# Performance work log

Measured on AMD Instinct MI355X. Metric: run time of the kernel, lower is better.

Reference implementation:

```python
import jax, jax.numpy as jnp
import numpy as np

EMBED = 768
HEADS = 12
HEAD_DIM = EMBED // HEADS
HIDDEN = 4 * EMBED
EPS = 1e-5


def _layernorm(x, g, b):
    mu = jnp.mean(x, axis=-1, keepdims=True)
    var = jnp.var(x, axis=-1, keepdims=True)
    return (x - mu) * jax.lax.rsqrt(var + EPS) * g + b


def setup_inputs() -> dict:
    key = jax.random.key(0)
    ks = jax.random.split(key, 12)
    s_e = 1.0 / np.sqrt(EMBED)
    s_h = 1.0 / np.sqrt(HIDDEN)
    return {
        "x": jax.random.normal(ks[0], (2, 2048, EMBED), dtype=jnp.float32),
        "ln1_g": jnp.ones((EMBED,), jnp.float32),
        "ln1_b": jnp.zeros((EMBED,), jnp.float32),
        "qkv_w": jax.random.uniform(ks[1], (EMBED, 3 * EMBED), jnp.float32, -s_e, s_e),
        "qkv_b": jax.random.uniform(ks[2], (3 * EMBED,), jnp.float32, -s_e, s_e),
        "proj_w": jax.random.uniform(ks[3], (EMBED, EMBED), jnp.float32, -s_e, s_e),
        "proj_b": jax.random.uniform(ks[4], (EMBED,), jnp.float32, -s_e, s_e),
        "ln2_g": jnp.ones((EMBED,), jnp.float32),
        "ln2_b": jnp.zeros((EMBED,), jnp.float32),
        "fc1_w": jax.random.uniform(ks[5], (EMBED, HIDDEN), jnp.float32, -s_e, s_e),
        "fc1_b": jax.random.uniform(ks[6], (HIDDEN,), jnp.float32, -s_e, s_e),
        "fc2_w": jax.random.uniform(ks[7], (HIDDEN, EMBED), jnp.float32, -s_h, s_h),
        "fc2_b": jax.random.uniform(ks[8], (EMBED,), jnp.float32, -s_h, s_h),
    }


def reference(x, ln1_g, ln1_b, qkv_w, qkv_b, proj_w, proj_b,
              ln2_g, ln2_b, fc1_w, fc1_b, fc2_w, fc2_b):
    B, L, C = x.shape
    scale = HEAD_DIM ** -0.5

    # --- attention sublayer (pre-LN) ---
    h = _layernorm(x, ln1_g, ln1_b)
    qkv = h @ qkv_w + qkv_b                       # [B, L, 3C]
    qkv = qkv.reshape(B, L, 3, HEADS, HEAD_DIM)
    q = jnp.transpose(qkv[:, :, 0], (0, 2, 1, 3))  # [B, H, L, D]
    k = jnp.transpose(qkv[:, :, 1], (0, 2, 1, 3))
    v = jnp.transpose(qkv[:, :, 2], (0, 2, 1, 3))
    attn = jnp.einsum('bhqd,bhkd->bhqk', q, k) * scale  # [B, H, L, L]
    attn = jax.nn.softmax(attn, axis=-1)
    out = jnp.einsum('bhqk,bhkd->bhqd', attn, v)  # [B, H, L, D]
    out = jnp.transpose(out, (0, 2, 1, 3)).reshape(B, L, C)
    x = x + (out @ proj_w + proj_b)

    # --- FFN sublayer (pre-LN) ---
    h = _layernorm(x, ln2_g, ln2_b)
    h = jax.nn.gelu(h @ fc1_w + fc1_b, approximate=False)
    x = x + (h @ fc2_w + fc2_b)
    return x
```

## Files before the change

kernel.cpp:

```cpp
#include <hip/hip_runtime.h>
#include <hip/hip_bf16.h>
#include <math.h>

#define EMBED   768
#define NHEADS  12
#define HD      64
#define HIDDEN  3072
#define SEQ     2048
#define BATCH   2
#define ROWS    (BATCH*SEQ)

#define QSCALE  0.1803368801111204f

typedef __bf16 bf16_t;
typedef __attribute__((ext_vector_type(8))) __bf16 bf16x8;
typedef __attribute__((ext_vector_type(4))) float f32x4;

static __device__ __forceinline__ f32x4 mfma16(bf16x8 a, bf16x8 b, f32x4 c) {
  return __builtin_amdgcn_mfma_f32_16x16x32_bf16(a, b, c, 0, 0, 0);
}

typedef __attribute__((address_space(1))) const void gas_void;
typedef __attribute__((address_space(3))) void las_void;
static __device__ __forceinline__ void gll16(const void* g, void* l) {
  __builtin_amdgcn_global_load_lds((gas_void*)g, (las_void*)l, 16, 0, 0);
}

__global__ __launch_bounds__(256) void ln_kernel(
    const float* __restrict__ x, const float* __restrict__ g,
    const float* __restrict__ bt, bf16_t* __restrict__ out)
{
  int row = blockIdx.x;
  int tid = threadIdx.x;
  const float* xr = x + (size_t)row * EMBED;
  float v0 = xr[tid], v1 = xr[tid + 256], v2 = xr[tid + 512];
  float s  = v0 + v1 + v2;
  float s2 = v0*v0 + v1*v1 + v2*v2;
  #pragma unroll
  for (int o = 32; o >= 1; o >>= 1) {
    s  += __shfl_xor(s,  o, 64);
    s2 += __shfl_xor(s2, o, 64);
  }
  __shared__ float red[8];
  int wave = tid >> 6, lane = tid & 63;
  if (lane == 0) { red[wave] = s; red[wave + 4] = s2; }
  __syncthreads();
  s  = red[0] + red[1] + red[2] + red[3];
  s2 = red[4] + red[5] + red[6] + red[7];
  float mu  = s * (1.0f / EMBED);
  float var = s2 * (1.0f / EMBED) - mu * mu;
  float rs  = rsqrtf(var + 1e-5f);
  bf16_t* orow = out + (size_t)row * EMBED;
  orow[tid]       = (bf16_t)((v0 - mu) * rs * g[tid]       + bt[tid]);
  orow[tid + 256] = (bf16_t)((v1 - mu) * rs * g[tid + 256] + bt[tid + 256]);
  orow[tid + 512] = (bf16_t)((v2 - mu) * rs * g[tid + 512] + bt[tid + 512]);
}

__global__ __launch_bounds__(256) void transpose_cast(
    const float* __restrict__ in, bf16_t* __restrict__ out, int R, int C)
{
  __shared__ float tile[32][33];
  int c0 = blockIdx.x * 32, r0 = blockIdx.y * 32;
  int tx = threadIdx.x & 31, ty = threadIdx.x >> 5;
  #pragma unroll
  for (int p = 0; p < 4; ++p) {
    int r = ty + p * 8;
    tile[r][tx] = in[(size_t)(r0 + r) * C + c0 + tx];
  }
  __syncthreads();
  #pragma unroll
  for (int p = 0; p < 4; ++p) {
    int cc = ty + p * 8;
    out[(size_t)(c0 + cc) * R + r0 + tx] = (bf16_t)tile[tx][cc];
  }
}

__global__ __launch_bounds__(256) void v_transpose(
    const bf16_t* __restrict__ qkv, bf16_t* __restrict__ vt)
{
  __shared__ bf16_t tile[64][68];
  int bh = blockIdx.y;
  int b = bh / NHEADS, h = bh % NHEADS;
  int l0 = blockIdx.x * 64;
  int t = threadIdx.x;
  int dx = (t & 15) * 4;
  int ly = t >> 4;
  #pragma unroll
  for (int p = 0; p < 4; ++p) {
    int l = ly + p * 16;
    const bf16_t* src = qkv + (size_t)(b * SEQ + l0 + l) * 2304 + 1536 + h * HD + dx;
    *(uint2*)&tile[l][dx] = *(const uint2*)src;
  }
  __syncthreads();
  int lx = (t & 15) * 4;
  int dy = t >> 4;
  #pragma unroll
  for (int p = 0; p < 4; ++p) {
    int d = dy + p * 16;
    union { bf16_t h4[4]; uint2 u; } tmp;
    #pragma unroll
    for (int i = 0; i < 4; ++i) tmp.h4[i] = tile[lx + i][d];
    *(uint2*)&vt[((size_t)bh * HD + d) * SEQ + l0 + lx] = tmp.u;
  }
}

template<int MODE, int BN>
__global__ __launch_bounds__(256) void gemm_kernel(
    const bf16_t* __restrict__ A, const bf16_t* __restrict__ WT,
    const float* __restrict__ bias, const float* __restrict__ res,
    void* __restrict__ outp, int N, int K)
{
  constexpr int JT = BN / 32;
  __shared__ bf16_t As[128 * 64];
  __shared__ bf16_t Bs[BN * 64];
  int tid = threadIdx.x;
  int lane = tid & 63, wave = tid >> 6;
  int l15 = lane & 15, quad = lane >> 4;
  int wm = wave >> 1, wn = wave & 1;

  int Nn = N / BN;
  int lin = blockIdx.x;
  int bm = (lin & 7) + 8 * ((lin >> 3) / Nn);
  int bn = (lin >> 3) % Nn;
  int m0 = bm * 128, n0 = bn * BN;

  f32x4 acc[4][JT];
  #pragma unroll
  for (int i = 0; i < 4; ++i)
    #pragma unroll
    for (int j = 0; j < JT; ++j)
      acc[i][j] = (f32x4){0.f, 0.f, 0.f, 0.f};

  int grow = lane >> 3;
  int gcol = ((lane & 7) ^ grow) * 8;
  const bf16_t* abase = A  + (size_t)(m0 + wave * 32 + grow) * K + gcol;
  const bf16_t* bbase = WT + (size_t)(n0 + wave * (BN / 4) + grow) * K + gcol;
  int swk = l15 & 7;

  for (int k0 = 0; k0 < K; k0 += 64) {
    #pragma unroll
    for (int a = 0; a < 4; ++a)
      gll16(abase + (size_t)a * 8 * K + k0, &As[(wave * 32 + a * 8) * 64]);
    #pragma unroll
    for (int a = 0; a < BN / 32; ++a)
      gll16(bbase + (size_t)a * 8 * K + k0, &Bs[(wave * (BN / 4) + a * 8) * 64]);
    __syncthreads();

    #pragma unroll
    for (int g = 0; g < 2; ++g) {
      bf16x8 af[4], bfr[JT];
      #pragma unroll
      for (int i = 0; i < 4; ++i)
        af[i] = *(const bf16x8*)
            &As[(wm * 64 + i * 16 + l15) * 64 + (((g * 4 + quad) ^ swk) * 8)];
      #pragma unroll
      for (int j = 0; j < JT; ++j)
        bfr[j] = *(const bf16x8*)
            &Bs[(wn * (BN / 2) + j * 16 + l15) * 64 + (((g * 4 + quad) ^ swk) * 8)];
      #pragma unroll
      for (int i = 0; i < 4; ++i)
        #pragma unroll
        for (int j = 0; j < JT; ++j)
          acc[i][j] = mfma16(af[i], bfr[j], acc[i][j]);
    }
    __syncthreads();
  }

  #pragma unroll
  for (int i = 0; i < 4; ++i) {
    int mbase = m0 + wm * 64 + i * 16 + quad * 4;
    #pragma unroll
    for (int j = 0; j < JT; ++j) {
      int n = n0 + wn * (BN / 2) + j * 16 + l15;
      float bn_ = bias[n];
      #pragma unroll
      for (int r = 0; r < 4; ++r) {
        size_t idx = (size_t)(mbase + r) * N + n;
        float v = acc[i][j][r] + bn_;
        if (MODE == 1) v = 0.5f * v * (1.0f + erff(v * 0.70710678118654752f));
        if (MODE == 3 && n < 768) v *= QSCALE;
        if (MODE == 2) {
          v += res[idx];
          ((float*)outp)[idx] = v;
        } else {
          ((bf16_t*)outp)[idx] = (bf16_t)v;
        }
      }
    }
  }
}

__global__ __launch_bounds__(256, 2) void attn_kernel(
    const bf16_t* __restrict__ qkv, const bf16_t* __restrict__ vt,
    bf16_t* __restrict__ attnout)
{
  __attribute__((aligned(16))) __shared__ bf16_t smem[4 * 8192 + 4 * 640];
  __shared__ float dsumf[4][64];

  int qt = blockIdx.x, h = blockIdx.y, b = blockIdx.z;
  int tid = threadIdx.x;
  int wave = tid >> 6, lane = tid & 63;
  int l15 = lane & 15, quad = lane >> 4;
  int q0 = qt * 64;
  int bh = b * NHEADS + h;

  bf16_t* wbase = smem + wave * 8192;
  bf16_t* pt    = smem + 32768 + wave * 640;

  bf16x8 bq[4][2];
  #pragma unroll
  for (int qi = 0; qi < 4; ++qi) {
    const bf16_t* qrow = qkv + (size_t)(b * SEQ + q0 + qi * 16 + l15) * 2304
                             + h * HD + quad * 8;
    bq[qi][0] = *(const bf16x8*)qrow;
    bq[qi][1] = *(const bf16x8*)(qrow + 32);
  }

  f32x4 accO[4][4];
  #pragma unroll
  for (int qi = 0; qi < 4; ++qi)
    #pragma unroll
    for (int t2 = 0; t2 < 4; ++t2)
      accO[qi][t2] = (f32x4){0.f, 0.f, 0.f, 0.f};
  float lpart[4] = {0.f, 0.f, 0.f, 0.f};

  int krow_l = lane >> 3;
  int kchunk = ((lane & 7) ^ krow_l) * 8;
  const bf16_t* ksrc0 = qkv + (size_t)(b * SEQ + wave * 32 + krow_l) * 2304
                            + 768 + h * HD + kchunk;
  int vrow_l = lane >> 2;
  int vchunk = ((lane & 3) ^ (vrow_l & 3)) * 8;
  const bf16_t* vsrc0 = vt + ((size_t)bh * HD + vrow_l) * SEQ + wave * 32 + vchunk;

  constexpr int NIT = SEQ / 128;

  {
    const bf16_t* ks = ksrc0;
    const bf16_t* vs = vsrc0;
    bf16_t* kb = wbase;
    bf16_t* vb = wbase + 2048;
    #pragma unroll
    for (int p = 0; p < 4; ++p) {
      gll16(ks + (size_t)(p * 8) * 2304, kb + p * 512);
      gll16(vs + (size_t)(p * 16) * SEQ, vb + p * 512);
    }
  }

  int cb = 0;
  for (int it = 0; it < NIT; ++it) {
    {
      int kvn = ((it + 1) & (NIT - 1)) * 128;
      const bf16_t* ks = ksrc0 + (size_t)kvn * 2304;
      const bf16_t* vs = vsrc0 + kvn;
      bf16_t* kb = wbase + (cb ^ 1) * 4096;
      bf16_t* vb = kb + 2048;
      #pragma unroll
      for (int p = 0; p < 4; ++p) {
        gll16(ks + (size_t)(p * 8) * 2304, kb + p * 512);
        gll16(vs + (size_t)(p * 16) * SEQ, vb + p * 512);
      }
    }
    __asm__ volatile("s_waitcnt vmcnt(8)" ::: "memory");

    const bf16_t* kb = wbase + cb * 4096;
    const bf16_t* vb = kb + 2048;

    bf16x8 ak[2][2];
    #pragma unroll
    for (int t = 0; t < 2; ++t)
      #pragma unroll
      for (int f = 0; f < 2; ++f)
        ak[t][f] = *(const bf16x8*)
            &kb[(t * 16 + l15) * 64 + (((f * 4 + quad) ^ (l15 & 7)) * 8)];

    bf16x8 bv[4];
    #pragma unroll
    for (int t2 = 0; t2 < 4; ++t2)
      bv[t2] = *(const bf16x8*)
          &vb[(t2 * 16 + l15) * 32 + ((quad ^ (l15 & 3)) * 8)];

    #pragma unroll
    for (int qi = 0; qi < 4; ++qi) {
      #pragma unroll
      for (int t = 0; t < 2; ++t) {
        f32x4 s = (f32x4){0.f, 0.f, 0.f, 0.f};
        s = mfma16(ak[t][0], bq[qi][0], s);
        s = mfma16(ak[t][1], bq[qi][1], s);
        union { bf16_t b4[4]; uint2 u; } pk;
        float ls = 0.f;
        #pragma unroll
        for (int r = 0; r < 4; ++r) {
          float pv = exp2f(s[r]);
          ls += pv;
          pk.b4[r] = (bf16_t)pv;
        }
        lpart[qi] += ls;
        *(uint2*)&pt[l15 * 40 + t * 16 + quad * 4] = pk.u;
      }
      bf16x8 ap = *(const bf16x8*)&pt[l15 * 40 + quad * 8];
      #pragma unroll
      for (int t2 = 0; t2 < 4; ++t2)
        accO[qi][t2] = mfma16(ap, bv[t2], accO[qi][t2]);
    }
    cb ^= 1;
  }

  #pragma unroll
  for (int qi = 0; qi < 4; ++qi) {
    float l = lpart[qi];
    l += __shfl_xor(l, 16, 64);
    l += __shfl_xor(l, 32, 64);
    if (quad == 0) dsumf[wave][qi * 16 + l15] = l;
  }
  __syncthreads();

  float* slabf = (float*)smem;
  int rq = lane >> 3;
  int d0 = (lane & 7) * 8;

  #pragma unroll
  for (int pass = 0; pass < 2; ++pass) {
    if (pass) __syncthreads();
    #pragma unroll
    for (int qi2 = 0; qi2 < 2; ++qi2) {
      int qi = pass * 2 + qi2;
      #pragma unroll
      for (int t2 = 0; t2 < 4; ++t2)
        #pragma unroll
        for (int r = 0; r < 4; ++r)
          slabf[wave * 2048 + (qi2 * 16 + quad * 4 + r) * 64 + t2 * 16 + l15]
              = accO[qi][t2][r];
    }
    __syncthreads();
    int q_loc = wave * 8 + rq;
    f32x4 o0 = (f32x4){0.f,0.f,0.f,0.f}, o1 = (f32x4){0.f,0.f,0.f,0.f};
    #pragma unroll
    for (int sw = 0; sw < 4; ++sw) {
      o0 += *(const f32x4*)&slabf[sw * 2048 + q_loc * 64 + d0];
      o1 += *(const f32x4*)&slabf[sw * 2048 + q_loc * 64 + d0 + 4];
    }
    int q_abs = pass * 32 + q_loc;
    float den = dsumf[0][q_abs] + dsumf[1][q_abs] + dsumf[2][q_abs] + dsumf[3][q_abs];
    float inv = 1.0f / den;
    bf16_t ob[8];
    #pragma unroll
    for (int j = 0; j < 4; ++j) {
      ob[j]     = (bf16_t)(o0[j] * inv);
      ob[j + 4] = (bf16_t)(o1[j] * inv);
    }
    *(uint4*)&attnout[(size_t)(b * SEQ + q0 + q_abs) * EMBED + h * HD + d0]
        = *(const uint4*)ob;
  }
}

extern "C" void kernel_launch(void* const* d_in, const int* in_sizes, int n_in,
                              void* d_out, int out_size, void* d_ws, size_t ws_size,
                              hipStream_t stream) {
  (void)in_sizes; (void)n_in; (void)out_size; (void)ws_size;
  const float* x      = (const float*)d_in[0];
  const float* ln1_g  = (const float*)d_in[1];
  const float* ln1_b  = (const float*)d_in[2];
  const float* qkv_w  = (const float*)d_in[3];
  const float* qkv_b  = (const float*)d_in[4];
  const float* proj_w = (const float*)d_in[5];
  const float* proj_b = (const float*)d_in[6];
  const float* ln2_g  = (const float*)d_in[7];
  const float* ln2_b  = (const float*)d_in[8];
  const float* fc1_w  = (const float*)d_in[9];
  const float* fc1_b  = (const float*)d_in[10];
  const float* fc2_w  = (const float*)d_in[11];
  const float* fc2_b  = (const float*)d_in[12];
  float* out = (float*)d_out;

  char* p = (char*)d_ws;
  bf16_t* wqkvT  = (bf16_t*)p; p += (size_t)2304 * 768 * 2;
  bf16_t* wprojT = (bf16_t*)p; p += (size_t)768 * 768 * 2;
  bf16_t* wfc1T  = (bf16_t*)p; p += (size_t)3072 * 768 * 2;
  bf16_t* wfc2T  = (bf16_t*)p; p += (size_t)768 * 3072 * 2;
  bf16_t* hbuf   = (bf16_t*)p; p += (size_t)ROWS * 768 * 2;
  bf16_t* qkv    = (bf16_t*)p;
  bf16_t* hid    = (bf16_t*)p; p += (size_t)ROWS * 3072 * 2;
  bf16_t* vt     = (bf16_t*)p; p += (size_t)BATCH * NHEADS * HD * SEQ * 2;
  bf16_t* attno  = (bf16_t*)p; p += (size_t)ROWS * 768 * 2;

  transpose_cast<<<dim3(2304/32, 768/32),  256, 0, stream>>>(qkv_w,  wqkvT,  768,  2304);
  transpose_cast<<<dim3(768/32,  768/32),  256, 0, stream>>>(proj_w, wprojT, 768,  768);
  transpose_cast<<<dim3(3072/32, 768/32),  256, 0, stream>>>(fc1_w,  wfc1T,  768,  3072);
  transpose_cast<<<dim3(768/32,  3072/32), 256, 0, stream>>>(fc2_w,  wfc2T,  3072, 768);

  ln_kernel<<<ROWS, 256, 0, stream>>>(x, ln1_g, ln1_b, hbuf);
  gemm_kernel<3,128><<<32 * (2304/128), 256, 0, stream>>>(
      hbuf, wqkvT, qkv_b, nullptr, qkv, 2304, 768);
  v_transpose<<<dim3(SEQ/64, BATCH*NHEADS), 256, 0, stream>>>(qkv, vt);
  attn_kernel<<<dim3(SEQ/64, NHEADS, BATCH), 256, 0, stream>>>(qkv, vt, attno);
  gemm_kernel<2,64><<<32 * (768/64), 256, 0, stream>>>(
      attno, wprojT, proj_b, x, out, 768, 768);

  ln_kernel<<<ROWS, 256, 0, stream>>>(out, ln2_g, ln2_b, hbuf);
  gemm_kernel<1,128><<<32 * (3072/128), 256, 0, stream>>>(
      hbuf, wfc1T, fc1_b, nullptr, hid, 3072, 768);
  gemm_kernel<2,64><<<32 * (768/64), 256, 0, stream>>>(
      hid, wfc2T, fc2_b, out, out, 768, 3072);
}
```

Measured before the change: 303.4 us.

## Double attention query tile, merge weight transposes, use fast exp2

The attention kernel now processes 128 queries per block instead of 64, so each K/V tile loaded into LDS serves twice as many queries and the grid shrinks to 384 blocks. The four weight transpose-cast launches are merged into one kernel that picks the matrix by block index, saving launch overhead. The softmax exponent uses the hardware exp2 builtin where available. The larger query tile doubles the accumulator and Q registers, which risks lower occupancy or spills, and the smaller grid may not fill all compute units.

Measured after the change: 299.4 us. No clear change (-1.3%).

```diff
diff --git a/kernel.cpp b/kernel.cpp
--- a/kernel.cpp
+++ b/kernel.cpp
@@ -19,6 +19,14 @@
 static __device__ __forceinline__ f32x4 mfma16(bf16x8 a, bf16x8 b, f32x4 c) {
   return __builtin_amdgcn_mfma_f32_16x16x32_bf16(a, b, c, 0, 0, 0);
 }
+
+#if __has_builtin(__builtin_amdgcn_exp2f)
+static __device__ __forceinline__ float fast_exp2(float x) {
+  return __builtin_amdgcn_exp2f(x);
+}
+#else
+static __device__ __forceinline__ float fast_exp2(float x) { return exp2f(x); }
+#endif
 
 typedef __attribute__((address_space(1))) const void gas_void;
 typedef __attribute__((address_space(3))) void las_void;
@@ -56,11 +64,20 @@
   orow[tid + 512] = (bf16_t)((v2 - mu) * rs * g[tid + 512] + bt[tid + 512]);
 }
 
-__global__ __launch_bounds__(256) void transpose_cast(
-    const float* __restrict__ in, bf16_t* __restrict__ out, int R, int C)
+__global__ __launch_bounds__(256) void transpose_all(
+    const float* __restrict__ w0, bf16_t* __restrict__ o0,
+    const float* __restrict__ w1, bf16_t* __restrict__ o1,
+    const float* __restrict__ w2, bf16_t* __restrict__ o2,
+    const float* __restrict__ w3, bf16_t* __restrict__ o3)
 {
   __shared__ float tile[32][33];
-  int c0 = blockIdx.x * 32, r0 = blockIdx.y * 32;
+  int lin = blockIdx.x;
+  const float* in; bf16_t* out; int R, C, bx, by;
+  if (lin < 1728)      { in = w0; out = o0; R = 768;  C = 2304; lin -= 0;    bx = lin % 72; by = lin / 72; }
+  else if (lin < 2304) { in = w1; out = o1; R = 768;  C = 768;  lin -= 1728; bx = lin % 24; by = lin / 24; }
+  else if (lin < 4608) { in = w2; out = o2; R = 768;  C = 3072; lin -= 2304; bx = lin % 96; by = lin / 96; }
+  else                 { in = w3; out = o3; R = 3072; C = 768;  lin -= 4608; bx = lin % 24; by = lin / 24; }
+  int c0 = bx * 32, r0 = by * 32;
   int tx = threadIdx.x & 31, ty = threadIdx.x >> 5;
   #pragma unroll
   for (int p = 0; p < 4; ++p) {
@@ -195,34 +212,35 @@
     bf16_t* __restrict__ attnout)
 {
   __attribute__((aligned(16))) __shared__ bf16_t smem[4 * 8192 + 4 * 640];
-  __shared__ float dsumf[4][64];
+  __shared__ float dsumf[4][128];
 
   int qt = blockIdx.x, h = blockIdx.y, b = blockIdx.z;
   int tid = threadIdx.x;
   int wave = tid >> 6, lane = tid & 63;
   int l15 = lane & 15, quad = lane >> 4;
-  int q0 = qt * 64;
+  int q0 = qt * 128;
   int bh = b * NHEADS + h;
 
   bf16_t* wbase = smem + wave * 8192;
   bf16_t* pt    = smem + 32768 + wave * 640;
 
-  bf16x8 bq[4][2];
-  #pragma unroll
-  for (int qi = 0; qi < 4; ++qi) {
+  bf16x8 bq[8][2];
+  #pragma unroll
+  for (int qi = 0; qi < 8; ++qi) {
     const bf16_t* qrow = qkv + (size_t)(b * SEQ + q0 + qi * 16 + l15) * 2304
                              + h * HD + quad * 8;
     bq[qi][0] = *(const bf16x8*)qrow;
     bq[qi][1] = *(const bf16x8*)(qrow + 32);
   }
-
-  f32x4 accO[4][4];
-  #pragma unroll
-  for (int qi = 0; qi < 4; ++qi)
+  __asm__ volatile("s_waitcnt vmcnt(0)" ::: "memory");
+
+  f32x4 accO[8][4];
+  #pragma unroll
+  for (int qi = 0; qi < 8; ++qi)
     #pragma unroll
     for (int t2 = 0; t2 < 4; ++t2)
       accO[qi][t2] = (f32x4){0.f, 0.f, 0.f, 0.f};
-  float lpart[4] = {0.f, 0.f, 0.f, 0.f};
+  float lpart[8] = {};
 
   int krow_l = lane >> 3;
   int kchunk = ((lane & 7) ^ krow_l) * 8;
@@ -235,14 +253,12 @@
   constexpr int NIT = SEQ / 128;
 
   {
-    const bf16_t* ks = ksrc0;
-    const bf16_t* vs = vsrc0;
     bf16_t* kb = wbase;
     bf16_t* vb = wbase + 2048;
     #pragma unroll
     for (int p = 0; p < 4; ++p) {
-      gll16(ks + (size_t)(p * 8) * 2304, kb + p * 512);
-      gll16(vs + (size_t)(p * 16) * SEQ, vb + p * 512);
+      gll16(ksrc0 + (size_t)(p * 8) * 2304, kb + p * 512);
+      gll16(vsrc0 + (size_t)(p * 16) * SEQ, vb + p * 512);
     }
   }
 
@@ -280,7 +296,7 @@
           &vb[(t2 * 16 + l15) * 32 + ((quad ^ (l15 & 3)) * 8)];
 
     #pragma unroll
-    for (int qi = 0; qi < 4; ++qi) {
+    for (int qi = 0; qi < 8; ++qi) {
       #pragma unroll
       for (int t = 0; t < 2; ++t) {
         f32x4 s = (f32x4){0.f, 0.f, 0.f, 0.f};
@@ -290,7 +306,7 @@
         float ls = 0.f;
         #pragma unroll
         for (int r = 0; r < 4; ++r) {
-          float pv = exp2f(s[r]);
+          float pv = fast_exp2(s[r]);
           ls += pv;
           pk.b4[r] = (bf16_t)pv;
         }
@@ -306,7 +322,7 @@
   }
 
   #pragma unroll
-  for (int qi = 0; qi < 4; ++qi) {
+  for (int qi = 0; qi < 8; ++qi) {
     float l = lpart[qi];
     l += __shfl_xor(l, 16, 64);
     l += __shfl_xor(l, 32, 64);
@@ -318,9 +334,7 @@
   int rq = lane >> 3;
   int d0 = (lane & 7) * 8;
 
-  #pragma unroll
-  for (int pass = 0; pass < 2; ++pass) {
-    if (pass) __syncthreads();
+  for (int pass = 0; pass < 4; ++pass) {
     #pragma unroll
     for (int qi2 = 0; qi2 < 2; ++qi2) {
       int qi = pass * 2 + qi2;
@@ -350,6 +364,7 @@
     }
     *(uint4*)&attnout[(size_t)(b * SEQ + q0 + q_abs) * EMBED + h * HD + d0]
         = *(const uint4*)ob;
+    if (pass < 3) __syncthreads();
   }
 }
 
@@ -383,16 +398,14 @@
   bf16_t* vt     = (bf16_t*)p; p += (size_t)BATCH * NHEADS * HD * SEQ * 2;
   bf16_t* attno  = (bf16_t*)p; p += (size_t)ROWS * 768 * 2;
 
-  transpose_cast<<<dim3(2304/32, 768/32),  256, 0, stream>>>(qkv_w,  wqkvT,  768,  2304);
-  transpose_cast<<<dim3(768/32,  768/32),  256, 0, stream>>>(proj_w, wprojT, 768,  768);
-  transpose_cast<<<dim3(3072/32, 768/32),  256, 0, stream>>>(fc1_w,  wfc1T,  768,  3072);
-  transpose_cast<<<dim3(768/32,  3072/32), 256, 0, stream>>>(fc2_w,  wfc2T,  3072, 768);
+  transpose_all<<<6912, 256, 0, stream>>>(qkv_w, wqkvT, proj_w, wprojT,
+                                          fc1_w, wfc1T, fc2_w, wfc2T);
 
   ln_kernel<<<ROWS, 256, 0, stream>>>(x, ln1_g, ln1_b, hbuf);
   gemm_kernel<3,128><<<32 * (2304/128), 256, 0, stream>>>(
       hbuf, wqkvT, qkv_b, nullptr, qkv, 2304, 768);
   v_transpose<<<dim3(SEQ/64, BATCH*NHEADS), 256, 0, stream>>>(qkv, vt);
-  attn_kernel<<<dim3(SEQ/64, NHEADS, BATCH), 256, 0, stream>>>(qkv, vt, attno);
+  attn_kernel<<<dim3(SEQ/128, NHEADS, BATCH), 256, 0, stream>>>(qkv, vt, attno);
   gemm_kernel<2,64><<<32 * (768/64), 256, 0, stream>>>(
       attno, wprojT, proj_b, x, out, 768, 768);
 
```
